# Performance work log

Hardware: AMD Instinct MI355X
Metric: run time of the kernel (lower is better)

## Reference

```python
import jax, jax.numpy as jnp
import numpy as np

T, V, D, L, H, F, R = 1024, 17, 1024, 2, 16, 4096, 32
DH = D // H
LORA_SCALE = 2.0  # lora_alpha / r = 64 / 32
MASK_ID = 16
NEG = jnp.float32(-1e9)


def setup_inputs() -> dict:
    key = jax.random.key(0)
    ks = iter(jax.random.split(key, 64))
    def p(shape, std):
        return jax.random.normal(next(ks), shape, jnp.float32) * std
    inp = {
        "packed_context": jax.random.randint(next(ks), (T,), 0, V),
        "cu_seq_lens": jnp.sort(jax.random.randint(next(ks), (5,), 0, T)),
        "max_seq_len": T,
        "row_coords": jax.random.randint(next(ks), (T,), 0, 64),
        "col_coords": jax.random.randint(next(ks), (T,), 0, 64),
        "num_diffusion_steps": 2,
        "E": p((V, D), 0.02),  # embed rows actually used: weight[:vocab_size]
    }
    shapes = {"q": (D, D), "k": (D, D), "v": (D, D), "o": (D, D),
              "g": (D, F), "u": (D, F), "d": (F, D)}
    for nm, (di, do) in shapes.items():
        inp["W" + nm] = p((L, di, do), di ** -0.5)  # frozen NF4 base weight (dequantized)
        inp["A" + nm] = p((L, di, R), di ** -0.5)   # LoRA A
        inp["B" + nm] = p((L, R, do), 0.01)          # LoRA B (nonzero for grad testing)
    inp["ln1"] = jnp.ones((L, D), jnp.float32)
    inp["ln2"] = jnp.ones((L, D), jnp.float32)
    inp["lnf"] = jnp.ones((D,), jnp.float32)
    return inp


def _rms(x, w):
    return x * jax.lax.rsqrt(jnp.mean(x * x, axis=-1, keepdims=True) + 1e-6) * w


def _lora(x, W, A, B):
    # fused base matmul + low-rank LoRA delta
    return x @ W + LORA_SCALE * ((x @ A) @ B)


def _denoise_step(soft, E, Wq, Aq, Bq, Wk, Ak, Bk, Wv, Av, Bv, Wo, Ao, Bo,
                  Wg, Ag, Bg, Wu, Au, Bu, Wd, Ad, Bd, ln1, ln2, lnf, causal_bias):
    # soft-token embedding: [T,V] @ [V,D]
    x = soft @ E
    inv_sqrt_dh = jnp.float32(1.0 / np.sqrt(DH))
    for l in range(L):
        h = _rms(x, ln1[l])
        q = _lora(h, Wq[l], Aq[l], Bq[l]).reshape(T, H, DH)
        k = _lora(h, Wk[l], Ak[l], Bk[l]).reshape(T, H, DH)
        v = _lora(h, Wv[l], Av[l], Bv[l]).reshape(T, H, DH)
        scores = jnp.einsum('qhd,khd->hqk', q, k) * inv_sqrt_dh + causal_bias
        att = jax.nn.softmax(scores, axis=-1)
        ctx = jnp.einsum('hqk,khd->qhd', att, v).reshape(T, D)
        x = x + _lora(ctx, Wo[l], Ao[l], Bo[l])
        h2 = _rms(x, ln2[l])
        ff = jax.nn.silu(_lora(h2, Wg[l], Ag[l], Bg[l])) * _lora(h2, Wu[l], Au[l], Bu[l])
        x = x + _lora(ff, Wd[l], Ad[l], Bd[l])
    logits = _rms(x, lnf) @ E.T  # tied head over the 17-token task vocab
    return jax.nn.softmax(logits, axis=-1)


def reference(packed_context, cu_seq_lens, max_seq_len, row_coords, col_coords,
              num_diffusion_steps, E, Wq, Aq, Bq, Wk, Ak, Bk, Wv, Av, Bv,
              Wo, Ao, Bo, Wg, Ag, Bg, Wu, Au, Bu, Wd, Ad, Bd, ln1, ln2, lnf):
    causal_bias = jnp.where(jnp.tril(jnp.ones((T, T), bool)), jnp.float32(0.0), NEG)
    is_prompt = (packed_context != MASK_ID)[:, None]  # [T,1]
    ctx_onehot = jax.nn.one_hot(packed_context, V, dtype=jnp.float32)
    soft = jnp.zeros((T, V), jnp.float32).at[:, MASK_ID].set(1.0)
    for _ in range(int(num_diffusion_steps)):
        refined = _denoise_step(soft, E, Wq, Aq, Bq, Wk, Ak, Bk, Wv, Av, Bv,
                                Wo, Ao, Bo, Wg, Ag, Bg, Wu, Au, Bu, Wd, Ad, Bd,
                                ln1, ln2, lnf, causal_bias)
        soft = jnp.where(is_prompt, ctx_onehot, refined)
    return jnp.argmax(soft, axis=-1)
```

## Files before the change

kernel.cpp:

```cpp
#include <hip/hip_runtime.h>
#include <hip/hip_bf16.h>

#define T_LEN 1024
#define D_DIM 1024
#define V_DIM 17
#define H_NUM 16
#define DH_DIM 64
#define F_DIM 4096
#define R_LORA 32
#define N_LAYERS 2
#define N_STEPS 2
#define MASK_ID 16
#define LORA_SCALE 2.0f

typedef __attribute__((ext_vector_type(8))) short bfx8;
typedef __attribute__((ext_vector_type(4))) float f32x4;

typedef unsigned short ushort_t;
typedef unsigned int uint_t;

#define AS1 __attribute__((address_space(1)))
#define AS3 __attribute__((address_space(3)))

__device__ __forceinline__ void gload16(const ushort_t* g, ushort_t* l) {
    __builtin_amdgcn_global_load_lds((const AS1 void*)(const void*)g,
                                     (AS3 void*)(void*)l, 16, 0, 0);
}

__device__ __forceinline__ ushort_t f2bf(float v) {
    __hip_bfloat16 h = __float2bfloat16(v);
    return __builtin_bit_cast(unsigned short, h);
}
__device__ __forceinline__ float bf2f(ushort_t u) {
    return __uint_as_float(((uint_t)u) << 16);
}
__device__ __forceinline__ void split4_store(float y0, float y1, float y2, float y3,
                                             ushort_t* __restrict__ hi, ushort_t* __restrict__ lo,
                                             size_t idx) {
    ushort_t h0 = f2bf(y0), h1 = f2bf(y1), h2 = f2bf(y2), h3 = f2bf(y3);
    ushort_t l0 = f2bf(y0 - bf2f(h0));
    ushort_t l1 = f2bf(y1 - bf2f(h1));
    ushort_t l2 = f2bf(y2 - bf2f(h2));
    ushort_t l3 = f2bf(y3 - bf2f(h3));
    uint2 hv, lv;
    hv.x = (uint_t)h0 | ((uint_t)h1 << 16);
    hv.y = (uint_t)h2 | ((uint_t)h3 << 16);
    lv.x = (uint_t)l0 | ((uint_t)l1 << 16);
    lv.y = (uint_t)l2 | ((uint_t)l3 << 16);
    *(uint2*)(hi + idx) = hv;
    *(uint2*)(lo + idx) = lv;
}

__global__ void init_soft_kernel(float* __restrict__ soft) {
    int idx = blockIdx.x * blockDim.x + threadIdx.x;
    if (idx < T_LEN * V_DIM) {
        soft[idx] = ((idx % V_DIM) == MASK_ID) ? 1.0f : 0.0f;
    }
}

__global__ __launch_bounds__(256) void embed_rms_split_kernel(
    const float* __restrict__ soft, const float* __restrict__ E,
    const float* __restrict__ w, float* __restrict__ x,
    ushort_t* __restrict__ hi, ushort_t* __restrict__ lo)
{
    const int t = blockIdx.x, tid = threadIdx.x;
    __shared__ float srow[V_DIM];
    __shared__ float red[4];
    if (tid < V_DIM) srow[tid] = soft[t * V_DIM + tid];
    __syncthreads();
    const int d0 = tid * 4;
    float4 acc = {0.f, 0.f, 0.f, 0.f};
    #pragma unroll
    for (int v = 0; v < V_DIM; v++) {
        float s = srow[v];
        float4 e = *(const float4*)(E + (size_t)v * D_DIM + d0);
        acc.x = fmaf(s, e.x, acc.x);
        acc.y = fmaf(s, e.y, acc.y);
        acc.z = fmaf(s, e.z, acc.z);
        acc.w = fmaf(s, e.w, acc.w);
    }
    size_t base = (size_t)t * D_DIM + d0;
    *(float4*)(x + base) = acc;
    float ss = acc.x * acc.x + acc.y * acc.y + acc.z * acc.z + acc.w * acc.w;
    const int lane = tid & 63, wv = tid >> 6;
    #pragma unroll
    for (int off = 32; off > 0; off >>= 1) ss += __shfl_xor(ss, off);
    if (lane == 0) red[wv] = ss;
    __syncthreads();
    ss = red[0] + red[1] + red[2] + red[3];
    const float r = 1.0f / sqrtf(ss * (1.0f / D_DIM) + 1e-6f);
    const float4 wv4 = *(const float4*)(w + d0);
    split4_store(acc.x * r * wv4.x, acc.y * r * wv4.y, acc.z * r * wv4.z, acc.w * r * wv4.w,
                 hi, lo, base);
}

__global__ __launch_bounds__(256) void fold_kernel(
    const float* __restrict__ W,
    const float* __restrict__ A,
    const float* __restrict__ Bm,
    ushort_t* __restrict__ oHi,
    ushort_t* __restrict__ oLo,
    int K, int N)
{
    const int l = blockIdx.z;
    W   += (size_t)l * K * N;
    A   += (size_t)l * K * R_LORA;
    Bm  += (size_t)l * R_LORA * N;
    oHi += (size_t)l * K * N;
    oLo += (size_t)l * K * N;
    __shared__ float Als[64][R_LORA + 1];
    __shared__ uint_t tile[64][65];
    const int tid = threadIdx.x;
    const int n0 = blockIdx.x * 64, k0 = blockIdx.y * 64;

    {
        const int row = tid >> 2, c0 = (tid & 3) * 8;
        const float* src = A + (size_t)(k0 + row) * R_LORA + c0;
        float4 a0 = *(const float4*)(src);
        float4 a1 = *(const float4*)(src + 4);
        Als[row][c0 + 0] = a0.x; Als[row][c0 + 1] = a0.y;
        Als[row][c0 + 2] = a0.z; Als[row][c0 + 3] = a0.w;
        Als[row][c0 + 4] = a1.x; Als[row][c0 + 5] = a1.y;
        Als[row][c0 + 6] = a1.z; Als[row][c0 + 7] = a1.w;
    }
    const int nl = tid & 63, kq = tid >> 6;
    float wreg[16];
    #pragma unroll
    for (int i = 0; i < 16; i++)
        wreg[i] = W[(size_t)(k0 + kq * 16 + i) * N + n0 + nl];
    float breg[R_LORA];
    #pragma unroll
    for (int r = 0; r < R_LORA; r++) breg[r] = Bm[(size_t)r * N + n0 + nl];
    __syncthreads();
    #pragma unroll
    for (int i = 0; i < 16; i++) {
        const int kl = kq * 16 + i;
        float acc = 0.f;
        #pragma unroll
        for (int r = 0; r < R_LORA; r++) acc = fmaf(Als[kl][r], breg[r], acc);
        float val = wreg[i] + LORA_SCALE * acc;
        ushort_t h = f2bf(val);
        tile[kl][nl] = ((uint_t)h << 16) | (uint_t)f2bf(val - bf2f(h));
    }
    __syncthreads();
    {
        const int nl2 = tid >> 2;
        const int kc0 = (tid & 3) * 16;
        ushort_t hb[16], lb[16];
        #pragma unroll
        for (int i = 0; i < 16; i++) {
            uint_t pk = tile[kc0 + i][nl2];
            hb[i] = (ushort_t)(pk >> 16);
            lb[i] = (ushort_t)(pk & 0xffffu);
        }
        size_t idx = (size_t)(n0 + nl2) * K + k0 + kc0;
        *(uint4*)(oHi + idx)     = *(uint4*)&hb[0];
        *(uint4*)(oHi + idx + 8) = *(uint4*)&hb[8];
        *(uint4*)(oLo + idx)     = *(uint4*)&lb[0];
        *(uint4*)(oLo + idx + 8) = *(uint4*)&lb[8];
    }
}

struct GemmJob {
    const ushort_t* Bh;
    const ushort_t* Bl;
    float* Cf;
    ushort_t* Ch;
    ushort_t* Cl;
    int k0, k1;
};

__global__ __launch_bounds__(256) void gemm128_kernel(
    const ushort_t* __restrict__ Ahi, const ushort_t* __restrict__ Alo,
    int K, int N, int kslices,
    GemmJob j0, GemmJob j1, GemmJob j2, GemmJob j3,
    GemmJob j4, GemmJob j5, GemmJob j6, GemmJob j7)
{
    GemmJob jb;
    int s;
    {
        const int z = blockIdx.z;
        const int ji = z / kslices;
        s = z - ji * kslices;
        if      (ji == 0) jb = j0; else if (ji == 1) jb = j1;
        else if (ji == 2) jb = j2; else if (ji == 3) jb = j3;
        else if (ji == 4) jb = j4; else if (ji == 5) jb = j5;
        else if (ji == 6) jb = j6; else jb = j7;
    }
    const int klen = (jb.k1 - jb.k0) / kslices;
    const int myk0 = jb.k0 + s * klen;
    const int myk1 = myk0 + klen;
    float* Cf = jb.Cf ? jb.Cf + (size_t)s * T_LEN * (size_t)N : nullptr;

    __shared__ ushort_t Ash[128][32];
    __shared__ ushort_t Asl[128][32];
    __shared__ ushort_t Bsh[128][32];
    __shared__ ushort_t Bsl[128][32];

    const int tid = threadIdx.x, lane = tid & 63, w = tid >> 6;
    const int l15 = lane & 15, lg = lane >> 4;
    const int m0 = blockIdx.y * 128, n0 = blockIdx.x * 128;
    const int wm = (w >> 1) * 64, wn = (w & 1) * 64;

    const int r0 = w * 32;
    const int rsub = lane >> 2;
    const int cs = lane & 3;
    const int csl = (cs ^ ((rsub >> 1) & 3)) * 8;
    const int rsl = (lg ^ ((l15 >> 1) & 3)) * 8;

    f32x4 acc[4][4];
    #pragma unroll
    for (int i = 0; i < 4; i++)
        #pragma unroll
        for (int j = 0; j < 4; j++) acc[i][j] = f32x4{0.f, 0.f, 0.f, 0.f};

    const size_t rowA = (size_t)(m0 + r0 + rsub) * K;
    const size_t rowB = (size_t)(n0 + r0 + rsub) * K;
    const size_t rstep = (size_t)16 * K;

    for (int kk = myk0; kk < myk1; kk += 32) {
        {
            const ushort_t* a0 = Ahi + rowA + kk + csl;
            const ushort_t* a1 = Alo + rowA + kk + csl;
            const ushort_t* b0 = jb.Bh + rowB + kk + csl;
            const ushort_t* b1 = jb.Bl + rowB + kk + csl;
            gload16(a0,         &Ash[r0][0]);
            gload16(a0 + rstep, &Ash[r0 + 16][0]);
            gload16(a1,         &Asl[r0][0]);
            gload16(a1 + rstep, &Asl[r0 + 16][0]);
            gload16(b0,         &Bsh[r0][0]);
            gload16(b0 + rstep, &Bsh[r0 + 16][0]);
            gload16(b1,         &Bsl[r0][0]);
            gload16(b1 + rstep, &Bsl[r0 + 16][0]);
        }
        __syncthreads();
        bfx8 bh[4], bl[4];
        #pragma unroll
        for (int ni = 0; ni < 4; ni++) {
            bh[ni] = *(const bfx8*)&Bsh[wn + ni * 16 + l15][rsl];
            bl[ni] = *(const bfx8*)&Bsl[wn + ni * 16 + l15][rsl];
        }
        #pragma unroll
        for (int mi = 0; mi < 4; mi++) {
            bfx8 ah = *(const bfx8*)&Ash[wm + mi * 16 + l15][rsl];
            bfx8 al = *(const bfx8*)&Asl[wm + mi * 16 + l15][rsl];
            #pragma unroll
            for (int ni = 0; ni < 4; ni++) {
                acc[mi][ni] = __builtin_amdgcn_mfma_f32_16x16x32_bf16(ah, bh[ni], acc[mi][ni], 0, 0, 0);
                acc[mi][ni] = __builtin_amdgcn_mfma_f32_16x16x32_bf16(ah, bl[ni], acc[mi][ni], 0, 0, 0);
                acc[mi][ni] = __builtin_amdgcn_mfma_f32_16x16x32_bf16(al, bh[ni], acc[mi][ni], 0, 0, 0);
            }
        }
        __syncthreads();
    }

    if (Cf) {
        #pragma unroll
        for (int mi = 0; mi < 4; mi++)
            #pragma unroll
            for (int ni = 0; ni < 4; ni++) {
                int col = n0 + wn + ni * 16 + l15;
                #pragma unroll
                for (int i = 0; i < 4; i++) {
                    int row = m0 + wm + mi * 16 + lg * 4 + i;
                    Cf[(size_t)row * N + col] = acc[mi][ni][i];
                }
            }
    } else {
        #pragma unroll
        for (int mi = 0; mi < 4; mi++)
            #pragma unroll
            for (int ni = 0; ni < 4; ni++) {
                int col = n0 + wn + ni * 16 + l15;
                #pragma unroll
                for (int i = 0; i < 4; i++) {
                    int row = m0 + wm + mi * 16 + lg * 4 + i;
                    size_t idx = (size_t)row * N + col;
                    float v = acc[mi][ni][i];
                    ushort_t h = f2bf(v);
                    jb.Ch[idx] = h;
                    jb.Cl[idx] = f2bf(v - bf2f(h));
                }
            }
    }
}

__global__ __launch_bounds__(256) void qkv_sum_split_kernel(
    const float* __restrict__ P, int S,
    ushort_t* __restrict__ qbh, ushort_t* __restrict__ qbl,
    ushort_t* __restrict__ kbh, ushort_t* __restrict__ kbl,
    ushort_t* __restrict__ vbh, ushort_t* __restrict__ vbl)
{
    const size_t DD1 = (size_t)T_LEN * D_DIM;
    size_t e = ((size_t)blockIdx.x * 256 + threadIdx.x) * 4;
    float4 q = {0,0,0,0}, k = {0,0,0,0}, v = {0,0,0,0};
    for (int j = 0; j < S; j++) {
        float4 a = *(const float4*)(P + (size_t)j * DD1 + e);
        q.x += a.x; q.y += a.y; q.z += a.z; q.w += a.w;
        float4 b = *(const float4*)(P + (size_t)(S + j) * DD1 + e);
        k.x += b.x; k.y += b.y; k.z += b.z; k.w += b.w;
        float4 c = *(const float4*)(P + (size_t)(2 * S + j) * DD1 + e);
        v.x += c.x; v.y += c.y; v.z += c.z; v.w += c.w;
    }
    split4_store(q.x, q.y, q.z, q.w, qbh, qbl, e);
    split4_store(k.x, k.y, k.z, k.w, kbh, kbl, e);
    split4_store(v.x, v.y, v.z, v.w, vbh, vbl, e);
}

__global__ void addn_kernel(float* __restrict__ x, const float* __restrict__ P,
                            int nparts, int n4) {
    int i = blockIdx.x * blockDim.x + threadIdx.x;
    if (i < n4) {
        const size_t DD1 = (size_t)T_LEN * D_DIM;
        size_t e = (size_t)i * 4;
        float4 xv = *(const float4*)(x + e);
        for (int j = 0; j < nparts; j++) {
            float4 p = *(const float4*)(P + (size_t)j * DD1 + e);
            xv.x += p.x; xv.y += p.y; xv.z += p.z; xv.w += p.w;
        }
        *(float4*)(x + e) = xv;
    }
}

__global__ __launch_bounds__(256) void add_rms_split_kernel(
    float* __restrict__ x, const float* __restrict__ P, int nparts,
    const float* __restrict__ w, ushort_t* __restrict__ hi, ushort_t* __restrict__ lo)
{
    const int t = blockIdx.x, tid = threadIdx.x;
    const size_t DD1 = (size_t)T_LEN * D_DIM;
    size_t base = (size_t)t * D_DIM + tid * 4;
    float4 xv = *(const float4*)(x + base);
    for (int j = 0; j < nparts; j++) {
        float4 p = *(const float4*)(P + (size_t)j * DD1 + base);
        xv.x += p.x; xv.y += p.y; xv.z += p.z; xv.w += p.w;
    }
    *(float4*)(x + base) = xv;
    float ss = xv.x * xv.x + xv.y * xv.y + xv.z * xv.z + xv.w * xv.w;
    __shared__ float red[4];
    const int lane = tid & 63, wv = tid >> 6;
    #pragma unroll
    for (int off = 32; off > 0; off >>= 1) ss += __shfl_xor(ss, off);
    if (lane == 0) red[wv] = ss;
    __syncthreads();
    ss = red[0] + red[1] + red[2] + red[3];
    const float r = 1.0f / sqrtf(ss * (1.0f / D_DIM) + 1e-6f);
    const float4 wv4 = *(const float4*)(w + tid * 4);
    split4_store(xv.x * r * wv4.x, xv.y * r * wv4.y, xv.z * r * wv4.z, xv.w * r * wv4.w,
                 hi, lo, base);
}

__global__ void silu_sum_split_kernel(const float* __restrict__ P, int parts,
                                      ushort_t* __restrict__ hi, ushort_t* __restrict__ lo) {
    const size_t DF1 = (size_t)T_LEN * F_DIM;
    size_t e = ((size_t)blockIdx.x * 256 + threadIdx.x) * 4;
    float4 g = {0,0,0,0}, u = {0,0,0,0};
    for (int j = 0; j < parts; j++) {
        float4 a = *(const float4*)(P + (size_t)j * DF1 + e);
        g.x += a.x; g.y += a.y; g.z += a.z; g.w += a.w;
        float4 b = *(const float4*)(P + (size_t)(parts + j) * DF1 + e);
        u.x += b.x; u.y += b.y; u.z += b.z; u.w += b.w;
    }
    float y0 = g.x / (1.f + expf(-g.x)) * u.x;
    float y1 = g.y / (1.f + expf(-g.y)) * u.y;
    float y2 = g.z / (1.f + expf(-g.z)) * u.z;
    float y3 = g.w / (1.f + expf(-g.w)) * u.w;
    split4_store(y0, y1, y2, y3, hi, lo, e);
}

#define KS_PAD 72
#define P_PAD 72
__global__ __launch_bounds__(256, 1) void attn_mfma_kernel(
    const ushort_t* __restrict__ qh, const ushort_t* __restrict__ ql,
    const ushort_t* __restrict__ kh, const ushort_t* __restrict__ kl,
    const ushort_t* __restrict__ vh, const ushort_t* __restrict__ vl,
    ushort_t* __restrict__ chi, ushort_t* __restrict__ clo)
{
    __shared__ ushort_t Ksh[64][KS_PAD];
    __shared__ ushort_t Ksl[64][KS_PAD];
    __shared__ ushort_t VTh[64][KS_PAD];
    __shared__ ushort_t VTl[64][KS_PAD];
    __shared__ ushort_t Ph[4][16][P_PAD];
    __shared__ ushort_t Pl[4][16][P_PAD];

    const int qt = blockIdx.x, hh = blockIdx.y;
    const int tid = threadIdx.x, w = tid >> 6, lane = tid & 63;
    const int l15 = lane & 15, lg = lane >> 4;
    const int q0 = qt * 64;
    const int hcol = hh * DH_DIM;

    bfx8 qa_h[2], qa_l[2];
    {
        size_t qrow = (size_t)(q0 + w * 16 + l15) * D_DIM + hcol;
        #pragma unroll
        for (int ks = 0; ks < 2; ks++) {
            qa_h[ks] = *(const bfx8*)(qh + qrow + ks * 32 + lg * 8);
            qa_l[ks] = *(const bfx8*)(ql + qrow + ks * 32 + lg * 8);
        }
    }

    f32x4 o[4];
    #pragma unroll
    for (int ni = 0; ni < 4; ni++) o[ni] = f32x4{0.f, 0.f, 0.f, 0.f};
    float mrun[4], lrun[4];
    #pragma unroll
    for (int i = 0; i < 4; i++) { mrun[i] = -3.0e38f; lrun[i] = 0.f; }

    const int srow = tid >> 2;
    const int sseg = (tid & 3) * 16;
    const int vp = tid & 31;
    const int vd0 = (tid >> 5) * 8;

    for (int kt = 0; kt <= qt; kt++) {
        __syncthreads();
        {
            size_t src = (size_t)(kt * 64 + srow) * D_DIM + hcol + sseg;
            *(uint4*)&Ksh[srow][sseg]     = *(const uint4*)(kh + src);
            *(uint4*)&Ksh[srow][sseg + 8] = *(const uint4*)(kh + src + 8);
            *(uint4*)&Ksl[srow][sseg]     = *(const uint4*)(kl + src);
            *(uint4*)&Ksl[srow][sseg + 8] = *(const uint4*)(kl + src + 8);
        }
        {
            size_t s0 = (size_t)(kt * 64 + 2 * vp) * D_DIM + hcol + vd0;
            uint4 h0 = *(const uint4*)(vh + s0);
            uint4 h1 = *(const uint4*)(vh + s0 + D_DIM);
            uint4 l0 = *(const uint4*)(vl + s0);
            uint4 l1 = *(const uint4*)(vl + s0 + D_DIM);
            const ushort_t* a = (const ushort_t*)&h0;
            const ushort_t* b = (const ushort_t*)&h1;
            const ushort_t* c = (const ushort_t*)&l0;
            const ushort_t* d = (const ushort_t*)&l1;
            #pragma unroll
            for (int j = 0; j < 8; j++) {
                *(uint_t*)&VTh[vd0 + j][2 * vp] = (uint_t)a[j] | ((uint_t)b[j] << 16);
                *(uint_t*)&VTl[vd0 + j][2 * vp] = (uint_t)c[j] | ((uint_t)d[j] << 16);
            }
        }
        __syncthreads();

        f32x4 s[4];
        #pragma unroll
        for (int ni = 0; ni < 4; ni++) s[ni] = f32x4{0.f, 0.f, 0.f, 0.f};
        #pragma unroll
        for (int ks = 0; ks < 2; ks++) {
            #pragma unroll
            for (int ni = 0; ni < 4; ni++) {
                bfx8 bh = *(const bfx8*)&Ksh[ni * 16 + l15][ks * 32 + lg * 8];
                bfx8 bl = *(const bfx8*)&Ksl[ni * 16 + l15][ks * 32 + lg * 8];
                s[ni] = __builtin_amdgcn_mfma_f32_16x16x32_bf16(qa_h[ks], bh, s[ni], 0, 0, 0);
                s[ni] = __builtin_amdgcn_mfma_f32_16x16x32_bf16(qa_h[ks], bl, s[ni], 0, 0, 0);
                s[ni] = __builtin_amdgcn_mfma_f32_16x16x32_bf16(qa_l[ks], bh, s[ni], 0, 0, 0);
            }
        }

        const int kbase = kt * 64;
        float rmax[4];
        #pragma unroll
        for (int i = 0; i < 4; i++) rmax[i] = -3.0e38f;
        #pragma unroll
        for (int ni = 0; ni < 4; ni++) {
            int kc = kbase + ni * 16 + l15;
            #pragma unroll
            for (int i = 0; i < 4; i++) {
                int qrow = q0 + w * 16 + lg * 4 + i;
                float v = s[ni][i] * 0.125f;
                v = (kc <= qrow) ? v : -3.0e38f;
                s[ni][i] = v;
                rmax[i] = fmaxf(rmax[i], v);
            }
        }
        #pragma unroll
        for (int off = 1; off < 16; off <<= 1) {
            #pragma unroll
            for (int i = 0; i < 4; i++) rmax[i] = fmaxf(rmax[i], __shfl_xor(rmax[i], off));
        }
        float psum[4];
        #pragma unroll
        for (int i = 0; i < 4; i++) {
            float nm = fmaxf(mrun[i], rmax[i]);
            float sc = __expf(mrun[i] - nm);
            lrun[i] *= sc;
            #pragma unroll
            for (int ni = 0; ni < 4; ni++) o[ni][i] *= sc;
            mrun[i] = nm;
            psum[i] = 0.f;
        }
        #pragma unroll
        for (int ni = 0; ni < 4; ni++) {
            #pragma unroll
            for (int i = 0; i < 4; i++) {
                float e = __expf(s[ni][i] - mrun[i]);
                s[ni][i] = e;
                psum[i] += e;
            }
        }
        #pragma unroll
        for (int off = 1; off < 16; off <<= 1) {
            #pragma unroll
            for (int i = 0; i < 4; i++) psum[i] += __shfl_xor(psum[i], off);
        }
        #pragma unroll
        for (int i = 0; i < 4; i++) lrun[i] += psum[i];

        #pragma unroll
        for (int ni = 0; ni < 4; ni++) {
            #pragma unroll
            for (int i = 0; i < 4; i++) {
                float e = s[ni][i];
                ushort_t hp = f2bf(e);
                Ph[w][lg * 4 + i][ni * 16 + l15] = hp;
                Pl[w][lg * 4 + i][ni * 16 + l15] = f2bf(e - bf2f(hp));
            }
        }
        #pragma unroll
        for (int ks = 0; ks < 2; ks++) {
            bfx8 ah = *(const bfx8*)&Ph[w][l15][ks * 32 + lg * 8];
            bfx8 al = *(const bfx8*)&Pl[w][l15][ks * 32 + lg * 8];
            #pragma unroll
            for (int ni = 0; ni < 4; ni++) {
                bfx8 bh = *(const bfx8*)&VTh[ni * 16 + l15][ks * 32 + lg * 8];
                bfx8 bl = *(const bfx8*)&VTl[ni * 16 + l15][ks * 32 + lg * 8];
                o[ni] = __builtin_amdgcn_mfma_f32_16x16x32_bf16(ah, bh, o[ni], 0, 0, 0);
                o[ni] = __builtin_amdgcn_mfma_f32_16x16x32_bf16(ah, bl, o[ni], 0, 0, 0);
                o[ni] = __builtin_amdgcn_mfma_f32_16x16x32_bf16(al, bh, o[ni], 0, 0, 0);
            }
        }
    }

    #pragma unroll
    for (int i = 0; i < 4; i++) {
        float inv = 1.0f / lrun[i];
        #pragma unroll
        for (int ni = 0; ni < 4; ni++) o[ni][i] *= inv;
    }
    #pragma unroll
    for (int ni = 0; ni < 4; ni++) {
        int col = hcol + ni * 16 + l15;
        #pragma unroll
        for (int i = 0; i < 4; i++) {
            int row = q0 + w * 16 + lg * 4 + i;
            size_t idx = (size_t)row * D_DIM + col;
            float v = o[ni][i];
            ushort_t hp = f2bf(v);
            chi[idx] = hp;
            clo[idx] = f2bf(v - bf2f(hp));
        }
    }
}

__global__ __launch_bounds__(256) void head_kernel(const float* __restrict__ x,
                                                   const float* __restrict__ lnf,
                                                   const float* __restrict__ E,
                                                   const int* __restrict__ tok,
                                                   float* __restrict__ soft) {
    int t = blockIdx.x;
    int tid = threadIdx.x;
    __shared__ float y[D_DIM];
    __shared__ float red[4];
    __shared__ float logits[V_DIM];
    const float* xr = x + (size_t)t * D_DIM;
    float ss = 0.f;
    for (int d = tid; d < D_DIM; d += 256) { float v = xr[d]; ss += v * v; }
    int lane = tid & 63, wave = tid >> 6;
    for (int off = 32; off > 0; off >>= 1) ss += __shfl_xor(ss, off);
    if (lane == 0) red[wave] = ss;
    __syncthreads();
    ss = red[0] + red[1] + red[2] + red[3];
    float r = 1.0f / sqrtf(ss * (1.0f / D_DIM) + 1e-6f);
    for (int d = tid; d < D_DIM; d += 256) y[d] = xr[d] * r * lnf[d];
    __syncthreads();
    for (int vv = wave; vv < V_DIM; vv += 4) {
        float p = 0.f;
        for (int d = lane; d < D_DIM; d += 64) p += y[d] * E[vv * D_DIM + d];
        for (int off = 32; off > 0; off >>= 1) p += __shfl_xor(p, off);
        if (lane == 0) logits[vv] = p;
    }
    __syncthreads();
    if (tid == 0) {
        int tk = tok[t];
        if (tk != MASK_ID) {
            for (int vv = 0; vv < V_DIM; vv++) soft[t * V_DIM + vv] = (vv == tk) ? 1.f : 0.f;
        } else {
            float mx = -1e30f;
            for (int vv = 0; vv < V_DIM; vv++) mx = fmaxf(mx, logits[vv]);
            float sm = 0.f;
            float e[V_DIM];
            for (int vv = 0; vv < V_DIM; vv++) { e[vv] = expf(logits[vv] - mx); sm += e[vv]; }
            float invs = 1.0f / sm;
            for (int vv = 0; vv < V_DIM; vv++) soft[t * V_DIM + vv] = e[vv] * invs;
        }
    }
}

__global__ void argmax_kernel(const float* __restrict__ soft, int* __restrict__ out) {
    int t = blockIdx.x * blockDim.x + threadIdx.x;
    if (t < T_LEN) {
        const float* s = soft + t * V_DIM;
        int best = 0;
        float bv = s[0];
        #pragma unroll
        for (int vv = 1; vv < V_DIM; vv++) {
            float v = s[vv];
            if (v > bv) { bv = v; best = vv; }
        }
        out[t] = best;
    }
}

__global__ __launch_bounds__(256) void rms_kernel(const float* __restrict__ x,
                                                  const float* __restrict__ w,
                                                  float* __restrict__ out) {
    int t = blockIdx.x;
    const float* xr = x + (size_t)t * D_DIM;
    float ss = 0.f;
    for (int d = threadIdx.x; d < D_DIM; d += 256) { float v = xr[d]; ss += v * v; }
    __shared__ float red[4];
    int lane = threadIdx.x & 63, wave = threadIdx.x >> 6;
    for (int off = 32; off > 0; off >>= 1) ss += __shfl_xor(ss, off);
    if (lane == 0) red[wave] = ss;
    __syncthreads();
    ss = red[0] + red[1] + red[2] + red[3];
    float r = 1.0f / sqrtf(ss * (1.0f / D_DIM) + 1e-6f);
    for (int d = threadIdx.x; d < D_DIM; d += 256) out[(size_t)t * D_DIM + d] = xr[d] * r * w[d];
}

__global__ __launch_bounds__(256) void embed_kernel(const float* __restrict__ soft,
                                                    const float* __restrict__ E,
                                                    float* __restrict__ x) {
    int t = blockIdx.x;
    __shared__ float srow[V_DIM];
    if (threadIdx.x < V_DIM) srow[threadIdx.x] = soft[t * V_DIM + threadIdx.x];
    __syncthreads();
    for (int d = threadIdx.x; d < D_DIM; d += 256) {
        float acc = 0.f;
        #pragma unroll
        for (int v = 0; v < V_DIM; v++) acc += srow[v] * E[v * D_DIM + d];
        x[(size_t)t * D_DIM + d] = acc;
    }
}

__global__ __launch_bounds__(256) void gemm_kernel(const float* __restrict__ A,
                                                   const float* __restrict__ B,
                                                   float* __restrict__ C,
                                                   int M, int N, int K,
                                                   float alpha, int accumulate) {
    const int BM = 64, BN = 64, BK = 16;
    __shared__ float As[BK][BM];
    __shared__ float Bsh[BK][BN];
    int tid = threadIdx.x;
    int tx = tid % 16, ty = tid / 16;
    int row0 = blockIdx.y * BM, col0 = blockIdx.x * BN;
    float acc[4][4] = {};
    for (int k0 = 0; k0 < K; k0 += BK) {
        #pragma unroll
        for (int i = 0; i < 4; i++) {
            int e = tid * 4 + i;
            int m = e / BK, kk = e % BK;
            int gr = row0 + m, gk = k0 + kk;
            As[kk][m] = (gr < M && gk < K) ? A[(size_t)gr * K + gk] : 0.f;
        }
        #pragma unroll
        for (int i = 0; i < 4; i++) {
            int e = tid * 4 + i;
            int kk = e / BN, n = e % BN;
            int gk = k0 + kk, gc = col0 + n;
            Bsh[kk][n] = (gk < K && gc < N) ? B[(size_t)gk * N + gc] : 0.f;
        }
        __syncthreads();
        #pragma unroll
        for (int kk = 0; kk < BK; kk++) {
            float a[4], b[4];
            #pragma unroll
            for (int i = 0; i < 4; i++) a[i] = As[kk][ty * 4 + i];
            #pragma unroll
            for (int j = 0; j < 4; j++) b[j] = Bsh[kk][tx * 4 + j];
            #pragma unroll
            for (int i = 0; i < 4; i++)
                #pragma unroll
                for (int j = 0; j < 4; j++)
                    acc[i][j] += a[i] * b[j];
        }
        __syncthreads();
    }
    #pragma unroll
    for (int i = 0; i < 4; i++) {
        int r = row0 + ty * 4 + i;
        if (r >= M) continue;
        #pragma unroll
        for (int j = 0; j < 4; j++) {
            int c = col0 + tx * 4 + j;
            if (c >= N) continue;
            size_t idx = (size_t)r * N + c;
            float val = alpha * acc[i][j];
            if (accumulate) val += C[idx];
            C[idx] = val;
        }
    }
}

__global__ __launch_bounds__(256) void attn_kernel(const float* __restrict__ q,
                                                   const float* __restrict__ k,
                                                   const float* __restrict__ v,
                                                   float* __restrict__ ctx) {
    int qi = blockIdx.x;
    int hh = blockIdx.y;
    __shared__ float sc[T_LEN];
    __shared__ float qrow[DH_DIM];
    __shared__ float red[8];
    __shared__ float part[4][DH_DIM];
    int tid = threadIdx.x;
    int lane = tid & 63, wave = tid >> 6;
    const float* qp = q + (size_t)qi * D_DIM + hh * DH_DIM;
    if (tid < DH_DIM) qrow[tid] = qp[tid];
    __syncthreads();
    const float scale = 0.125f;
    for (int j = wave; j <= qi; j += 4) {
        const float* kp = k + (size_t)j * D_DIM + hh * DH_DIM;
        float p = qrow[lane] * kp[lane];
        for (int off = 32; off > 0; off >>= 1) p += __shfl_xor(p, off);
        if (lane == 0) sc[j] = p * scale;
    }
    __syncthreads();
    int n = qi + 1;
    float m = -1e30f;
    for (int j = tid; j < n; j += 256) m = fmaxf(m, sc[j]);
    for (int off = 32; off > 0; off >>= 1) m = fmaxf(m, __shfl_xor(m, off));
    if (lane == 0) red[wave] = m;
    __syncthreads();
    m = fmaxf(fmaxf(red[0], red[1]), fmaxf(red[2], red[3]));
    float s = 0.f;
    for (int j = tid; j < n; j += 256) { float e = expf(sc[j] - m); sc[j] = e; s += e; }
    for (int off = 32; off > 0; off >>= 1) s += __shfl_xor(s, off);
    if (lane == 0) red[4 + wave] = s;
    __syncthreads();
    s = red[4] + red[5] + red[6] + red[7];
    float inv = 1.0f / s;
    float acc = 0.f;
    for (int j = wave; j < n; j += 4) {
        acc += sc[j] * v[(size_t)j * D_DIM + hh * DH_DIM + lane];
    }
    part[wave][lane] = acc;
    __syncthreads();
    if (tid < DH_DIM) {
        float r = (part[0][tid] + part[1][tid] + part[2][tid] + part[3][tid]) * inv;
        ctx[(size_t)qi * D_DIM + hh * DH_DIM + tid] = r;
    }
}

__global__ void silu_mul_kernel(const float* __restrict__ g, const float* __restrict__ u,
                                float* __restrict__ out, int nelem) {
    int i = blockIdx.x * blockDim.x + threadIdx.x;
    if (i < nelem) {
        float gv = g[i];
        float sg = 1.0f / (1.0f + expf(-gv));
        out[i] = gv * sg * u[i];
    }
}

static inline void launch_gemm(const float* A, const float* B, float* C,
                               int M, int N, int K, float alpha, int accumulate,
                               hipStream_t stream) {
    dim3 grid((N + 63) / 64, (M + 63) / 64);
    gemm_kernel<<<grid, 256, 0, stream>>>(A, B, C, M, N, K, alpha, accumulate);
}

extern "C" void kernel_launch(void* const* d_in, const int* in_sizes, int n_in,
                              void* d_out, int out_size, void* d_ws, size_t ws_size,
                              hipStream_t stream) {
    const int* packed = (const int*)d_in[0];
    const float* E  = (const float*)d_in[6];
    const float* Wsrc[7] = {(const float*)d_in[7],  (const float*)d_in[10], (const float*)d_in[13],
                            (const float*)d_in[16], (const float*)d_in[19], (const float*)d_in[22],
                            (const float*)d_in[25]};
    const float* Asrc[7] = {(const float*)d_in[8],  (const float*)d_in[11], (const float*)d_in[14],
                            (const float*)d_in[17], (const float*)d_in[20], (const float*)d_in[23],
                            (const float*)d_in[26]};
    const float* Bsrc[7] = {(const float*)d_in[9],  (const float*)d_in[12], (const float*)d_in[15],
                            (const float*)d_in[18], (const float*)d_in[21], (const float*)d_in[24],
                            (const float*)d_in[27]};
    const float* ln1 = (const float*)d_in[28];
    const float* ln2 = (const float*)d_in[29];
    const float* lnf = (const float*)d_in[30];

    const size_t DD = (size_t)D_DIM * D_DIM;
    const size_t DF = (size_t)D_DIM * F_DIM;
    const size_t wsizes[7] = {DD, DD, DD, DD, DF, DF, DF};
    const int Kdim[7] = {D_DIM, D_DIM, D_DIM, D_DIM, D_DIM, D_DIM, F_DIM};
    const int Ndim[7] = {D_DIM, D_DIM, D_DIM, D_DIM, F_DIM, F_DIM, D_DIM};

    size_t u16_elems = 0;
    for (int p = 0; p < 7; p++) u16_elems += 2ull * N_LAYERS * wsizes[p];
    u16_elems += 2ull * DD;
    u16_elems += 2ull * DD;
    u16_elems += 2ull * DF;
    u16_elems += 6ull * DD;
    size_t f32_mid = (size_t)T_LEN * V_DIM + DD + 8 * DD;
    size_t f32_big = (size_t)T_LEN * V_DIM + DD + 16 * DD;
    size_t need_mid = u16_elems * 2 + f32_mid * 4 + 256;
    size_t need_big = u16_elems * 2 + f32_big * 4 + 256;

    if (ws_size >= need_mid) {
        const bool big = (ws_size >= need_big);
        ushort_t* ub = (ushort_t*)d_ws;
        size_t uo = 0;
        ushort_t *Whi[7], *Wlo[7];
        for (int p = 0; p < 7; p++) {
            Whi[p] = ub + uo; uo += (size_t)N_LAYERS * wsizes[p];
            Wlo[p] = ub + uo; uo += (size_t)N_LAYERS * wsizes[p];
        }
        ushort_t* h_hi = ub + uo; uo += DD;
        ushort_t* h_lo = ub + uo; uo += DD;
        ushort_t* c_hi = ub + uo; uo += DD;
        ushort_t* c_lo = ub + uo; uo += DD;
        ushort_t* f_hi = ub + uo; uo += DF;
        ushort_t* f_lo = ub + uo; uo += DF;
        ushort_t* qbh = ub + uo; uo += DD;
        ushort_t* qbl = ub + uo; uo += DD;
        ushort_t* kbh = ub + uo; uo += DD;
        ushort_t* kbl = ub + uo; uo += DD;
        ushort_t* vbh = ub + uo; uo += DD;
        ushort_t* vbl = ub + uo; uo += DD;
        float* fb = (float*)(ub + uo);
        size_t fo = 0;
        float* soft = fb + fo; fo += (size_t)T_LEN * V_DIM;
        float* x    = fb + fo; fo += DD;
        float* P    = fb + fo;

        for (int p = 0; p < 7; p++) {
            dim3 grid(Ndim[p] / 64, Kdim[p] / 64, N_LAYERS);
            fold_kernel<<<grid, 256, 0, stream>>>(Wsrc[p], Asrc[p], Bsrc[p],
                                                  Whi[p], Wlo[p], Kdim[p], Ndim[p]);
        }

        init_soft_kernel<<<(T_LEN * V_DIM + 255) / 256, 256, 0, stream>>>(soft);

        const int n4 = (int)(DD / 4);
        const int qkvS = big ? 4 : 2;
        const int dprS = big ? 16 : 8;
        const int guS  = big ? 2 : 1;
        GemmJob jz = {};

        for (int step = 0; step < N_STEPS; step++) {
            embed_rms_split_kernel<<<T_LEN, 256, 0, stream>>>(soft, E, ln1, x, h_hi, h_lo);
            for (int l = 0; l < N_LAYERS; l++) {
                {
                    GemmJob jq = {Whi[0] + l * DD, Wlo[0] + l * DD, P,                      nullptr, nullptr, 0, D_DIM};
                    GemmJob jk = {Whi[1] + l * DD, Wlo[1] + l * DD, P + (size_t)qkvS * DD,  nullptr, nullptr, 0, D_DIM};
                    GemmJob jv = {Whi[2] + l * DD, Wlo[2] + l * DD, P + (size_t)2 * qkvS * DD, nullptr, nullptr, 0, D_DIM};
                    gemm128_kernel<<<dim3(8, 8, 3 * qkvS), 256, 0, stream>>>(
                        h_hi, h_lo, D_DIM, D_DIM, qkvS, jq, jk, jv, jz, jz, jz, jz, jz);
                    qkv_sum_split_kernel<<<(int)(DD / 4 / 256), 256, 0, stream>>>(
                        P, qkvS, qbh, qbl, kbh, kbl, vbh, vbl);
                }
                attn_mfma_kernel<<<dim3(T_LEN / 64, H_NUM), 256, 0, stream>>>(
                    qbh, qbl, kbh, kbl, vbh, vbl, c_hi, c_lo);
                {
                    GemmJob jo = {Whi[3] + l * DD, Wlo[3] + l * DD, P, nullptr, nullptr, 0, D_DIM};
                    gemm128_kernel<<<dim3(8, 8, 8), 256, 0, stream>>>(
                        c_hi, c_lo, D_DIM, D_DIM, 8, jo, jz, jz, jz, jz, jz, jz, jz);
                    add_rms_split_kernel<<<T_LEN, 256, 0, stream>>>(
                        x, P, 8, ln2 + (size_t)l * D_DIM, h_hi, h_lo);
                }
                {
                    GemmJob jg = {Whi[4] + l * DF, Wlo[4] + l * DF, P,                     nullptr, nullptr, 0, D_DIM};
                    GemmJob ju = {Whi[5] + l * DF, Wlo[5] + l * DF, P + (size_t)guS * DF,  nullptr, nullptr, 0, D_DIM};
                    gemm128_kernel<<<dim3(32, 8, 2 * guS), 256, 0, stream>>>(
                        h_hi, h_lo, D_DIM, F_DIM, guS, jg, ju, jz, jz, jz, jz, jz, jz);
                    silu_sum_split_kernel<<<(int)(DF / 4 / 256), 256, 0, stream>>>(
                        P, guS, f_hi, f_lo);
                }
                {
                    GemmJob jd = {Whi[6] + l * DF, Wlo[6] + l * DF, P, nullptr, nullptr, 0, F_DIM};
                    gemm128_kernel<<<dim3(8, 8, dprS), 256, 0, stream>>>(
                        f_hi, f_lo, F_DIM, D_DIM, dprS, jd, jz, jz, jz, jz, jz, jz, jz);
                    if (l + 1 < N_LAYERS) {
                        add_rms_split_kernel<<<T_LEN, 256, 0, stream>>>(
                            x, P, dprS, ln1 + (size_t)(l + 1) * D_DIM, h_hi, h_lo);
                    } else {
                        addn_kernel<<<(n4 + 255) / 256, 256, 0, stream>>>(x, P, dprS, n4);
                    }
                }
            }
            head_kernel<<<T_LEN, 256, 0, stream>>>(x, lnf, E, packed, soft);
        }
        argmax_kernel<<<(T_LEN + 255) / 256, 256, 0, stream>>>(soft, (int*)d_out);
        return;
    }

    float* ws = (float*)d_ws;
    size_t off = 0;
    float* soft = ws + off; off += (size_t)T_LEN * V_DIM;
    float* x    = ws + off; off += (size_t)T_LEN * D_DIM;
    float* h    = ws + off; off += (size_t)T_LEN * D_DIM;
    float* qb   = ws + off; off += (size_t)T_LEN * D_DIM;
    float* kb   = ws + off; off += (size_t)T_LEN * D_DIM;
    float* vb   = ws + off; off += (size_t)T_LEN * D_DIM;
    float* cb   = ws + off; off += (size_t)T_LEN * D_DIM;
    float* gb   = ws + off; off += (size_t)T_LEN * F_DIM;
    float* ubf  = ws + off; off += (size_t)T_LEN * F_DIM;
    float* tmp  = ws + off; off += (size_t)T_LEN * R_LORA;

    init_soft_kernel<<<(T_LEN * V_DIM + 255) / 256, 256, 0, stream>>>(soft);
    for (int step = 0; step < N_STEPS; step++) {
        embed_kernel<<<T_LEN, 256, 0, stream>>>(soft, E, x);
        for (int l = 0; l < N_LAYERS; l++) {
            const float* ln1_l = ln1 + (size_t)l * D_DIM;
            const float* ln2_l = ln2 + (size_t)l * D_DIM;
            rms_kernel<<<T_LEN, 256, 0, stream>>>(x, ln1_l, h);
            launch_gemm(h, Asrc[0] + (size_t)l * D_DIM * R_LORA, tmp, T_LEN, R_LORA, D_DIM, 1.0f, 0, stream);
            launch_gemm(h, Wsrc[0] + (size_t)l * DD, qb, T_LEN, D_DIM, D_DIM, 1.0f, 0, stream);
            launch_gemm(tmp, Bsrc[0] + (size_t)l * R_LORA * D_DIM, qb, T_LEN, D_DIM, R_LORA, LORA_SCALE, 1, stream);
            launch_gemm(h, Asrc[1] + (size_t)l * D_DIM * R_LORA, tmp, T_LEN, R_LORA, D_DIM, 1.0f, 0, stream);
            launch_gemm(h, Wsrc[1] + (size_t)l * DD, kb, T_LEN, D_DIM, D_DIM, 1.0f, 0, stream);
            launch_gemm(tmp, Bsrc[1] + (size_t)l * R_LORA * D_DIM, kb, T_LEN, D_DIM, R_LORA, LORA_SCALE, 1, stream);
            launch_gemm(h, Asrc[2] + (size_t)l * D_DIM * R_LORA, tmp, T_LEN, R_LORA, D_DIM, 1.0f, 0, stream);
            launch_gemm(h, Wsrc[2] + (size_t)l * DD, vb, T_LEN, D_DIM, D_DIM, 1.0f, 0, stream);
            launch_gemm(tmp, Bsrc[2] + (size_t)l * R_LORA * D_DIM, vb, T_LEN, D_DIM, R_LORA, LORA_SCALE, 1, stream);
            attn_kernel<<<dim3(T_LEN, H_NUM), 256, 0, stream>>>(qb, kb, vb, cb);
            launch_gemm(cb, Asrc[3] + (size_t)l * D_DIM * R_LORA, tmp, T_LEN, R_LORA, D_DIM, 1.0f, 0, stream);
            launch_gemm(cb, Wsrc[3] + (size_t)l * DD, x, T_LEN, D_DIM, D_DIM, 1.0f, 1, stream);
            launch_gemm(tmp, Bsrc[3] + (size_t)l * R_LORA * D_DIM, x, T_LEN, D_DIM, R_LORA, LORA_SCALE, 1, stream);
            rms_kernel<<<T_LEN, 256, 0, stream>>>(x, ln2_l, h);
            launch_gemm(h, Asrc[4] + (size_t)l * D_DIM * R_LORA, tmp, T_LEN, R_LORA, D_DIM, 1.0f, 0, stream);
            launch_gemm(h, Wsrc[4] + (size_t)l * DF, gb, T_LEN, F_DIM, D_DIM, 1.0f, 0, stream);
            launch_gemm(tmp, Bsrc[4] + (size_t)l * R_LORA * F_DIM, gb, T_LEN, F_DIM, R_LORA, LORA_SCALE, 1, stream);
            launch_gemm(h, Asrc[5] + (size_t)l * D_DIM * R_LORA, tmp, T_LEN, R_LORA, D_DIM, 1.0f, 0, stream);
            launch_gemm(h, Wsrc[5] + (size_t)l * DF, ubf, T_LEN, F_DIM, D_DIM, 1.0f, 0, stream);
            launch_gemm(tmp, Bsrc[5] + (size_t)l * R_LORA * F_DIM, ubf, T_LEN, F_DIM, R_LORA, LORA_SCALE, 1, stream);
            silu_mul_kernel<<<(T_LEN * F_DIM + 255) / 256, 256, 0, stream>>>(gb, ubf, gb, T_LEN * F_DIM);
            launch_gemm(gb, Asrc[6] + (size_t)l * F_DIM * R_LORA, tmp, T_LEN, R_LORA, F_DIM, 1.0f, 0, stream);
            launch_gemm(gb, Wsrc[6] + (size_t)l * DF, x, T_LEN, D_DIM, F_DIM, 1.0f, 1, stream);
            launch_gemm(tmp, Bsrc[6] + (size_t)l * R_LORA * D_DIM, x, T_LEN, D_DIM, R_LORA, LORA_SCALE, 1, stream);
        }
        head_kernel<<<T_LEN, 256, 0, stream>>>(x, lnf, E, packed, soft);
    }
    argmax_kernel<<<(T_LEN + 255) / 256, 256, 0, stream>>>(soft, (int*)d_out);
}
```

Baseline: 1.201 ms.

## Double-buffer GEMM LDS tiles, prefetch attention K/V, reduce split-K slices

The GEMM kernel gets two LDS buffers so the next K-tile's global-to-LDS loads are issued while MFMAs run on the current tile. The attention kernel keeps the next K/V tile in registers, loading it after the LDS write so the memory latency overlaps compute. The split-K factors are fixed lower (qkv 2, o-proj 4, gate/up 1, down 8), and the large-workspace path is removed. This cuts partial-sum traffic and reduction work, but it gives fewer blocks per launch and doubles LDS use in the GEMM, which may lower occupancy.

Measured after the change: 1.034 ms. -13.9%, faster.

```diff
diff --git a/kernel.cpp b/kernel.cpp
--- a/kernel.cpp
+++ b/kernel.cpp
@@ -192,10 +192,10 @@
     const int myk1 = myk0 + klen;
     float* Cf = jb.Cf ? jb.Cf + (size_t)s * T_LEN * (size_t)N : nullptr;
 
-    __shared__ ushort_t Ash[128][32];
-    __shared__ ushort_t Asl[128][32];
-    __shared__ ushort_t Bsh[128][32];
-    __shared__ ushort_t Bsl[128][32];
+    __shared__ ushort_t Ash[2][128][32];
+    __shared__ ushort_t Asl[2][128][32];
+    __shared__ ushort_t Bsh[2][128][32];
+    __shared__ ushort_t Bsl[2][128][32];
 
     const int tid = threadIdx.x, lane = tid & 63, w = tid >> 6;
     const int l15 = lane & 15, lg = lane >> 4;
@@ -218,32 +218,36 @@
     const size_t rowB = (size_t)(n0 + r0 + rsub) * K;
     const size_t rstep = (size_t)16 * K;
 
+    auto stage = [&](int b, int kk) {
+        const ushort_t* a0 = Ahi + rowA + kk + csl;
+        const ushort_t* a1 = Alo + rowA + kk + csl;
+        const ushort_t* b0 = jb.Bh + rowB + kk + csl;
+        const ushort_t* b1 = jb.Bl + rowB + kk + csl;
+        gload16(a0,         &Ash[b][r0][0]);
+        gload16(a0 + rstep, &Ash[b][r0 + 16][0]);
+        gload16(a1,         &Asl[b][r0][0]);
+        gload16(a1 + rstep, &Asl[b][r0 + 16][0]);
+        gload16(b0,         &Bsh[b][r0][0]);
+        gload16(b0 + rstep, &Bsh[b][r0 + 16][0]);
+        gload16(b1,         &Bsl[b][r0][0]);
+        gload16(b1 + rstep, &Bsl[b][r0 + 16][0]);
+    };
+
+    stage(0, myk0);
+    __syncthreads();
+    int cur = 0;
     for (int kk = myk0; kk < myk1; kk += 32) {
-        {
-            const ushort_t* a0 = Ahi + rowA + kk + csl;
-            const ushort_t* a1 = Alo + rowA + kk + csl;
-            const ushort_t* b0 = jb.Bh + rowB + kk + csl;
-            const ushort_t* b1 = jb.Bl + rowB + kk + csl;
-            gload16(a0,         &Ash[r0][0]);
-            gload16(a0 + rstep, &Ash[r0 + 16][0]);
-            gload16(a1,         &Asl[r0][0]);
-            gload16(a1 + rstep, &Asl[r0 + 16][0]);
-            gload16(b0,         &Bsh[r0][0]);
-            gload16(b0 + rstep, &Bsh[r0 + 16][0]);
-            gload16(b1,         &Bsl[r0][0]);
-            gload16(b1 + rstep, &Bsl[r0 + 16][0]);
-        }
-        __syncthreads();
+        if (kk + 32 < myk1) stage(cur ^ 1, kk + 32);
         bfx8 bh[4], bl[4];
         #pragma unroll
         for (int ni = 0; ni < 4; ni++) {
-            bh[ni] = *(const bfx8*)&Bsh[wn + ni * 16 + l15][rsl];
-            bl[ni] = *(const bfx8*)&Bsl[wn + ni * 16 + l15][rsl];
+            bh[ni] = *(const bfx8*)&Bsh[cur][wn + ni * 16 + l15][rsl];
+            bl[ni] = *(const bfx8*)&Bsl[cur][wn + ni * 16 + l15][rsl];
         }
         #pragma unroll
         for (int mi = 0; mi < 4; mi++) {
-            bfx8 ah = *(const bfx8*)&Ash[wm + mi * 16 + l15][rsl];
-            bfx8 al = *(const bfx8*)&Asl[wm + mi * 16 + l15][rsl];
+            bfx8 ah = *(const bfx8*)&Ash[cur][wm + mi * 16 + l15][rsl];
+            bfx8 al = *(const bfx8*)&Asl[cur][wm + mi * 16 + l15][rsl];
             #pragma unroll
             for (int ni = 0; ni < 4; ni++) {
                 acc[mi][ni] = __builtin_amdgcn_mfma_f32_16x16x32_bf16(ah, bh[ni], acc[mi][ni], 0, 0, 0);
@@ -252,6 +256,7 @@
             }
         }
         __syncthreads();
+        cur ^= 1;
     }
 
     if (Cf) {
@@ -410,25 +415,32 @@
     const int vp = tid & 31;
     const int vd0 = (tid >> 5) * 8;
 
+    uint4 kh0, kh1, kl0, kl1, vh0, vh1, vl0, vl1;
+    auto load_tile = [&](int kt) {
+        size_t src = (size_t)(kt * 64 + srow) * D_DIM + hcol + sseg;
+        kh0 = *(const uint4*)(kh + src);
+        kh1 = *(const uint4*)(kh + src + 8);
+        kl0 = *(const uint4*)(kl + src);
+        kl1 = *(const uint4*)(kl + src + 8);
+        size_t s0 = (size_t)(kt * 64 + 2 * vp) * D_DIM + hcol + vd0;
+        vh0 = *(const uint4*)(vh + s0);
+        vh1 = *(const uint4*)(vh + s0 + D_DIM);
+        vl0 = *(const uint4*)(vl + s0);
+        vl1 = *(const uint4*)(vl + s0 + D_DIM);
+    };
+    load_tile(0);
+
     for (int kt = 0; kt <= qt; kt++) {
         __syncthreads();
         {
-            size_t src = (size_t)(kt * 64 + srow) * D_DIM + hcol + sseg;
-            *(uint4*)&Ksh[srow][sseg]     = *(const uint4*)(kh + src);
-            *(uint4*)&Ksh[srow][sseg + 8] = *(const uint4*)(kh + src + 8);
-            *(uint4*)&Ksl[srow][sseg]     = *(const uint4*)(kl + src);
-            *(uint4*)&Ksl[srow][sseg + 8] = *(const uint4*)(kl + src + 8);
-        }
-        {
-            size_t s0 = (size_t)(kt * 64 + 2 * vp) * D_DIM + hcol + vd0;
-            uint4 h0 = *(const uint4*)(vh + s0);
-            uint4 h1 = *(const uint4*)(vh + s0 + D_DIM);
-            uint4 l0 = *(const uint4*)(vl + s0);
-            uint4 l1 = *(const uint4*)(vl + s0 + D_DIM);
-            const ushort_t* a = (const ushort_t*)&h0;
-            const ushort_t* b = (const ushort_t*)&h1;
-            const ushort_t* c = (const ushort_t*)&l0;
-            const ushort_t* d = (const ushort_t*)&l1;
+            *(uint4*)&Ksh[srow][sseg]     = kh0;
+            *(uint4*)&Ksh[srow][sseg + 8] = kh1;
+            *(uint4*)&Ksl[srow][sseg]     = kl0;
+            *(uint4*)&Ksl[srow][sseg + 8] = kl1;
+            const ushort_t* a = (const ushort_t*)&vh0;
+            const ushort_t* b = (const ushort_t*)&vh1;
+            const ushort_t* c = (const ushort_t*)&vl0;
+            const ushort_t* d = (const ushort_t*)&vl1;
             #pragma unroll
             for (int j = 0; j < 8; j++) {
                 *(uint_t*)&VTh[vd0 + j][2 * vp] = (uint_t)a[j] | ((uint_t)b[j] << 16);
@@ -436,6 +448,7 @@
             }
         }
         __syncthreads();
+        if (kt < qt) load_tile(kt + 1);
 
         f32x4 s[4];
         #pragma unroll
@@ -793,13 +806,10 @@
     u16_elems += 2ull * DD;
     u16_elems += 2ull * DF;
     u16_elems += 6ull * DD;
-    size_t f32_mid = (size_t)T_LEN * V_DIM + DD + 8 * DD;
-    size_t f32_big = (size_t)T_LEN * V_DIM + DD + 16 * DD;
-    size_t need_mid = u16_elems * 2 + f32_mid * 4 + 256;
-    size_t need_big = u16_elems * 2 + f32_big * 4 + 256;
-
-    if (ws_size >= need_mid) {
-        const bool big = (ws_size >= need_big);
+    size_t f32_elems = (size_t)T_LEN * V_DIM + DD + 8 * DD;
+    size_t need = u16_elems * 2 + f32_elems * 4 + 256;
+
+    if (ws_size >= need) {
         ushort_t* ub = (ushort_t*)d_ws;
         size_t uo = 0;
         ushort_t *Whi[7], *Wlo[7];
@@ -834,49 +844,46 @@
         init_soft_kernel<<<(T_LEN * V_DIM + 255) / 256, 256, 0, stream>>>(soft);
 
         const int n4 = (int)(DD / 4);
-        const int qkvS = big ? 4 : 2;
-        const int dprS = big ? 16 : 8;
-        const int guS  = big ? 2 : 1;
         GemmJob jz = {};
 
         for (int step = 0; step < N_STEPS; step++) {
             embed_rms_split_kernel<<<T_LEN, 256, 0, stream>>>(soft, E, ln1, x, h_hi, h_lo);
             for (int l = 0; l < N_LAYERS; l++) {
                 {
-                    GemmJob jq = {Whi[0] + l * DD, Wlo[0] + l * DD, P,                      nullptr, nullptr, 0, D_DIM};
-                    GemmJob jk = {Whi[1] + l * DD, Wlo[1] + l * DD, P + (size_t)qkvS * DD,  nullptr, nullptr, 0, D_DIM};
-                    GemmJob jv = {Whi[2] + l * DD, Wlo[2] + l * DD, P + (size_t)2 * qkvS * DD, nullptr, nullptr, 0, D_DIM};
-                    gemm128_kernel<<<dim3(8, 8, 3 * qkvS), 256, 0, stream>>>(
-                        h_hi, h_lo, D_DIM, D_DIM, qkvS, jq, jk, jv, jz, jz, jz, jz, jz);
+                    GemmJob jq = {Whi[0] + l * DD, Wlo[0] + l * DD, P,          nullptr, nullptr, 0, D_DIM};
+                    GemmJob jk = {Whi[1] + l * DD, Wlo[1] + l * DD, P + 2 * DD, nullptr, nullptr, 0, D_DIM};
+                    GemmJob jv = {Whi[2] + l * DD, Wlo[2] + l * DD, P + 4 * DD, nullptr, nullptr, 0, D_DIM};
+                    gemm128_kernel<<<dim3(8, 8, 6), 256, 0, stream>>>(
+                        h_hi, h_lo, D_DIM, D_DIM, 2, jq, jk, jv, jz, jz, jz, jz, jz);
                     qkv_sum_split_kernel<<<(int)(DD / 4 / 256), 256, 0, stream>>>(
-                        P, qkvS, qbh, qbl, kbh, kbl, vbh, vbl);
+                        P, 2, qbh, qbl, kbh, kbl, vbh, vbl);
                 }
                 attn_mfma_kernel<<<dim3(T_LEN / 64, H_NUM), 256, 0, stream>>>(
                     qbh, qbl, kbh, kbl, vbh, vbl, c_hi, c_lo);
                 {
                     GemmJob jo = {Whi[3] + l * DD, Wlo[3] + l * DD, P, nullptr, nullptr, 0, D_DIM};
-                    gemm128_kernel<<<dim3(8, 8, 8), 256, 0, stream>>>(
-                        c_hi, c_lo, D_DIM, D_DIM, 8, jo, jz, jz, jz, jz, jz, jz, jz);
+                    gemm128_kernel<<<dim3(8, 8, 4), 256, 0, stream>>>(
+                        c_hi, c_lo, D_DIM, D_DIM, 4, jo, jz, jz, jz, jz, jz, jz, jz);
                     add_rms_split_kernel<<<T_LEN, 256, 0, stream>>>(
-                        x, P, 8, ln2 + (size_t)l * D_DIM, h_hi, h_lo);
+                        x, P, 4, ln2 + (size_t)l * D_DIM, h_hi, h_lo);
                 }
                 {
-                    GemmJob jg = {Whi[4] + l * DF, Wlo[4] + l * DF, P,                     nullptr, nullptr, 0, D_DIM};
-                    GemmJob ju = {Whi[5] + l * DF, Wlo[5] + l * DF, P + (size_t)guS * DF,  nullptr, nullptr, 0, D_DIM};
-                    gemm128_kernel<<<dim3(32, 8, 2 * guS), 256, 0, stream>>>(
-                        h_hi, h_lo, D_DIM, F_DIM, guS, jg, ju, jz, jz, jz, jz, jz, jz);
+                    GemmJob jg = {Whi[4] + l * DF, Wlo[4] + l * DF, P,      nullptr, nullptr, 0, D_DIM};
+                    GemmJob ju = {Whi[5] + l * DF, Wlo[5] + l * DF, P + DF, nullptr, nullptr, 0, D_DIM};
+                    gemm128_kernel<<<dim3(32, 8, 2), 256, 0, stream>>>(
+                        h_hi, h_lo, D_DIM, F_DIM, 1, jg, ju, jz, jz, jz, jz, jz, jz);
                     silu_sum_split_kernel<<<(int)(DF / 4 / 256), 256, 0, stream>>>(
-                        P, guS, f_hi, f_lo);
+                        P, 1, f_hi, f_lo);
                 }
                 {
                     GemmJob jd = {Whi[6] + l * DF, Wlo[6] + l * DF, P, nullptr, nullptr, 0, F_DIM};
-                    gemm128_kernel<<<dim3(8, 8, dprS), 256, 0, stream>>>(
-                        f_hi, f_lo, F_DIM, D_DIM, dprS, jd, jz, jz, jz, jz, jz, jz, jz);
+                    gemm128_kernel<<<dim3(8, 8, 8), 256, 0, stream>>>(
+                        f_hi, f_lo, F_DIM, D_DIM, 8, jd, jz, jz, jz, jz, jz, jz, jz);
                     if (l + 1 < N_LAYERS) {
                         add_rms_split_kernel<<<T_LEN, 256, 0, stream>>>(
-                            x, P, dprS, ln1 + (size_t)(l + 1) * D_DIM, h_hi, h_lo);
+                            x, P, 8, ln1 + (size_t)(l + 1) * D_DIM, h_hi, h_lo);
                     } else {
-                        addn_kernel<<<(n4 + 255) / 256, 256, 0, stream>>>(x, P, dprS, n4);
+                        addn_kernel<<<(n4 + 255) / 256, 256, 0, stream>>>(x, P, 8, n4);
                     }
                 }
             }
```
